# Performance work log

Hardware: AMD Instinct MI355X
Metric: run time of the kernel (lower is better)

## Reference

```python
import jax, jax.numpy as jnp
import numpy as np
import math

D_MODEL = 1024
N_HEADS = 16
HEAD_DIM = D_MODEL // N_HEADS
MAX_CONTEXT_LEN = 512


def _alibi_slopes(n_heads):
    def pow2_slopes(n):
        start = 2.0 ** (-(2.0 ** (-(math.log2(n) - 3))))
        return [start * (start ** i) for i in range(n)]
    if math.log2(n_heads).is_integer():
        slopes = pow2_slopes(n_heads)
    else:
        closest = 2 ** math.floor(math.log2(n_heads))
        slopes = pow2_slopes(closest)
        slopes += pow2_slopes(2 * closest)[0::2][: n_heads - closest]
    return jnp.asarray(slopes, dtype=jnp.float32)


def setup_inputs() -> dict:
    key = jax.random.key(0)
    ks = jax.random.split(key, 9)
    B, L, D = 4, 2048, D_MODEL
    s = 1.0 / math.sqrt(D)
    inp = {
        "x": jax.random.normal(ks[0], (B, L, D), dtype=jnp.float32),
        "key_padding_mask": jnp.zeros((B, L), dtype=bool),
        "Wq": jax.random.normal(ks[1], (D, D), dtype=jnp.float32) * s,
        "bq": jnp.zeros((D,), dtype=jnp.float32),
        "Wk": jax.random.normal(ks[2], (D, D), dtype=jnp.float32) * s,
        "bk": jnp.zeros((D,), dtype=jnp.float32),
        "Wv": jax.random.normal(ks[3], (D, D), dtype=jnp.float32) * s,
        "bv": jnp.zeros((D,), dtype=jnp.float32),
        "Wo": jax.random.normal(ks[4], (D, D), dtype=jnp.float32) * s,
        "bo": jnp.zeros((D,), dtype=jnp.float32),
    }
    return inp


def _attn(x, key_padding_mask, Wq, bq, Wk, bk, Wv, bv, Wo, bo):
    B, L, D = x.shape
    H, d = N_HEADS, HEAD_DIM
    # projections (torch Linear: x @ W.T + b)
    q = (x @ Wq.T + bq).reshape(B, L, H, d)
    k = (x @ Wk.T + bk).reshape(B, L, H, d)
    v = (x @ Wv.T + bv).reshape(B, L, H, d)
    scores = jnp.einsum("bihd,bjhd->bhij", q, k) / math.sqrt(d)  # (B,H,L,L)
    # ALiBi bias: slope[h] * (j - i)
    i = jnp.arange(L)[:, None]
    j = jnp.arange(L)[None, :]
    slopes = _alibi_slopes(H).astype(scores.dtype)
    scores = scores + slopes[None, :, None, None] * (j - i).astype(scores.dtype)
    # causal + sliding-window mask
    mask = (j > i) | (j < i - MAX_CONTEXT_LEN)
    neg_inf = jnp.asarray(-jnp.inf, dtype=scores.dtype)
    scores = jnp.where(mask[None, None, :, :], neg_inf, scores)
    scores = jnp.where(key_padding_mask[:, None, None, :], neg_inf, scores)
    attn = jax.nn.softmax(scores, axis=-1)
    out = jnp.einsum("bhij,bjhd->bihd", attn, v).reshape(B, L, D)
    return out @ Wo.T + bo


def reference(x, key_padding_mask, Wq, bq, Wk, bk, Wv, bv, Wo, bo):
    return _attn(x, key_padding_mask, Wq, bq, Wk, bk, Wv, bv, Wo, bo)
```

## Files before the change

kernel.cpp:

```cpp
#include <hip/hip_runtime.h>
#include <stdint.h>

typedef __attribute__((ext_vector_type(8))) short bf16x8;
typedef __attribute__((ext_vector_type(4))) short s16x4;
typedef __attribute__((ext_vector_type(4))) float f32x4;

#define MFMA_BF16(A, B, C) __builtin_amdgcn_mfma_f32_16x16x32_bf16((A), (B), (C), 0, 0, 0)

__device__ __forceinline__ float bf2f(short u) {
  union { unsigned u32; float f; } c; c.u32 = ((unsigned)(unsigned short)u) << 16; return c.f;
}
__device__ __forceinline__ short f2bf(float f) {
  union { float f; unsigned u32; } c; c.f = f;
  unsigned u = c.u32;
  return (short)((u + 0x7fffu + ((u >> 16) & 1u)) >> 16);
}
__device__ __forceinline__ short f2bf_t(float f) {
  union { float f; unsigned u32; } c; c.f = f;
  return (short)(c.u32 >> 16);
}

#define NEG_BIG (-30000.0f)

__device__ __forceinline__ void async16(const void* g, void* l) {
  __builtin_amdgcn_global_load_lds(
      (__attribute__((address_space(1))) void*)(g),
      (__attribute__((address_space(3))) void*)(l), 16, 0, 0);
}

__global__ void __launch_bounds__(256) convert_kernel(
    const float* __restrict__ X,
    const float* __restrict__ W0, const float* __restrict__ W1,
    const float* __restrict__ W2, const float* __restrict__ W3,
    const float* __restrict__ B0, const float* __restrict__ B1,
    const float* __restrict__ B2, const float* __restrict__ B3,
    short* __restrict__ Xb, short* __restrict__ Wb, short* __restrict__ bb)
{
  long c = (long)blockIdx.x * 256 + threadIdx.x;
  const float* src; short* dst; long off;
  if (c < 2097152) {
    src = X; dst = Xb; off = c * 4;
  } else if (c < 3145728) {
    long u = c - 2097152; int w = (int)(u >> 18);
    src = (w == 0) ? W0 : (w == 1) ? W1 : (w == 2) ? W2 : W3;
    dst = Wb + (long)w * 1048576; off = (u & 262143) * 4;
  } else {
    long u = c - 3145728; int w = (int)(u >> 8);
    src = (w == 0) ? B0 : (w == 1) ? B1 : (w == 2) ? B2 : B3;
    dst = bb + w * 1024; off = (u & 255) * 4;
  }
  float4 v = *(const float4*)(src + off);
  s16x4 o; o[0] = f2bf(v.x); o[1] = f2bf(v.y); o[2] = f2bf(v.z); o[3] = f2bf(v.w);
  *(s16x4*)(dst + off) = o;
}

#define STAGE_B(PG2, KK)                                                     \
  {                                                                          \
    short* sb_ = lds + (PG2) + PA + wave * 512;                              \
    async16(gB + (KK), sb_);                                                 \
    async16(gB + 65536 + (KK), sb_ + 2048);                                  \
  }
#define STAGE_A(PG2, KK)                                                     \
  {                                                                          \
    short* sa_ = lds + (PG2) + wave * 512;                                   \
    _Pragma("unroll")                                                        \
    for (int q = 0; q < AR; ++q)                                             \
      async16(gA + (long)q * 65536 + (KK), sa_ + q * 2048);                  \
  }
#define KTILE(PG, PG2, STG, KK2, VM)                                         \
  {                                                                          \
    const short* pa_ = lds + (PG);                                           \
    const short* pb_ = pa_ + PA;                                             \
    _Pragma("unroll")                                                        \
    for (int m = 0; m < MT; ++m) {                                           \
      int rA = wr * (MT * 16) + m * 16 + ml;                                 \
      af[m] = *(const bf16x8*)(pa_ + rA * 32 + sl);                          \
    }                                                                        \
    _Pragma("unroll")                                                        \
    for (int n = 0; n < 4; ++n) {                                            \
      int rB = wcn * 64 + n * 16 + ml;                                       \
      bf[n] = *(const bf16x8*)(pb_ + rB * 32 + sl);                          \
    }                                                                        \
    if (STG) { STAGE_B(PG2, KK2) STAGE_A(PG2, KK2) }                         \
    __builtin_amdgcn_s_setprio(1);                                           \
    _Pragma("unroll")                                                        \
    for (int m = 0; m < MT; ++m)                                             \
      _Pragma("unroll")                                                      \
      for (int n = 0; n < 4; ++n)                                            \
        acc[m][n] = MFMA_BF16(af[m], bf[n], acc[m][n]);                      \
    __builtin_amdgcn_s_setprio(0);                                           \
    if constexpr ((VM) == 1) {                                               \
      if constexpr (MT == 8)                                                 \
        asm volatile("s_waitcnt vmcnt(6)" ::: "memory");                     \
      else                                                                   \
        asm volatile("s_waitcnt vmcnt(4)" ::: "memory");                     \
    } else if constexpr ((VM) == 2) {                                        \
      asm volatile("s_waitcnt vmcnt(0)" ::: "memory");                       \
    }                                                                        \
    if constexpr ((VM) != 0) {                                               \
      __builtin_amdgcn_s_barrier();                                          \
      __builtin_amdgcn_sched_barrier(0);                                     \
    }                                                                        \
  }

template <int MODE, int MT>
__device__ __forceinline__ void gemm_body(
    short* __restrict__ lds,
    const short* __restrict__ A, const short* __restrict__ W,
    const short* __restrict__ bias, void* __restrict__ C,
    float scale, int row0, int col0)
{
  constexpr int PA   = MT * 1024;
  constexpr int PAGE = PA + 4096;
  constexpr int AR   = MT / 2;

  const int tid  = threadIdx.x;
  const int lane = tid & 63;
  const int wave = tid >> 6;
  const int wr   = wave >> 1;
  const int wcn  = wave & 1;
  const int ml = lane & 15, quad = lane >> 4;

  f32x4 acc[MT][4];
  const f32x4 zero = {0.f, 0.f, 0.f, 0.f};
#pragma unroll
  for (int i = 0; i < MT; ++i)
#pragma unroll
    for (int j = 0; j < 4; ++j) acc[i][j] = zero;

  const int r_l = tid >> 2;
  const int c_l = (tid & 3) ^ ((r_l >> 1) & 3);
  const short* gA = A + (long)(row0 + r_l) * 1024 + c_l * 8;
  const short* gB = W + (long)(col0 + r_l) * 1024 + c_l * 8;

  const int sl = (quad ^ ((ml >> 1) & 3)) << 3;

  bf16x8 af[MT], bf[4];

  STAGE_A(0, 0) STAGE_B(0, 0)
  STAGE_A(PAGE, 32) STAGE_B(PAGE, 32)
  if constexpr (MT == 8) asm volatile("s_waitcnt vmcnt(6)" ::: "memory");
  else                   asm volatile("s_waitcnt vmcnt(4)" ::: "memory");
  __builtin_amdgcn_s_barrier();
  __builtin_amdgcn_sched_barrier(0);

  for (int t = 0; t < 30; t += 3) {
    const long k2 = (long)(t + 2) * 32;
    KTILE(0,        2 * PAGE, true, k2,      1)
    KTILE(PAGE,     0,        true, k2 + 32, 1)
    KTILE(2 * PAGE, PAGE,     true, k2 + 64, 1)
  }
  KTILE(0,    0, false, 0, 2)
  KTILE(PAGE, 0, false, 0, 0)

  const int ccol = col0 + wcn * 64;
  float bv4[4];
#pragma unroll
  for (int nt = 0; nt < 4; ++nt) bv4[nt] = bf2f(bias[ccol + nt * 16 + ml]);

  if (MODE == 2) {
    const int b = row0 >> 11;
    short* Vt = (short*)C;
#pragma unroll
    for (int mt = 0; mt < MT; ++mt) {
      int rr = row0 + wr * (MT * 16) + mt * 16 + quad * 4;
      int tloc = rr & 2047;
#pragma unroll
      for (int nt = 0; nt < 4; ++nt) {
        int cc = ccol + nt * 16 + ml;
        int h = cc >> 6, d = cc & 63;
        s16x4 pack;
#pragma unroll
        for (int r = 0; r < 4; ++r) pack[r] = f2bf(acc[mt][nt][r] + bv4[nt]);
        *(s16x4*)(Vt + (long)(b * 16 + h) * 131072 + (long)d * 2048 + tloc) = pack;
      }
    }
  } else {
#pragma unroll
    for (int mt = 0; mt < MT; ++mt) {
      int rr = row0 + wr * (MT * 16) + mt * 16 + quad * 4;
#pragma unroll
      for (int nt = 0; nt < 4; ++nt) {
        int cc = ccol + nt * 16 + ml;
#pragma unroll
        for (int r = 0; r < 4; ++r) {
          float v = (acc[mt][nt][r] + bv4[nt]) * scale;
          long idx = (long)(rr + r) * 1024 + cc;
          if (MODE == 1) ((float*)C)[idx] = v;
          else           ((short*)C)[idx] = f2bf(v);
        }
      }
    }
  }
}
#undef KTILE
#undef STAGE_A
#undef STAGE_B

__global__ void __launch_bounds__(256, 2) qkv_kernel(
    const short* __restrict__ Xb, const short* __restrict__ Wb,
    const short* __restrict__ bb,
    short* __restrict__ Q, short* __restrict__ K, short* __restrict__ Vt,
    float qscale)
{
  __shared__ __align__(16) short lds[36864];
  const int z = blockIdx.z;
  const short* W = Wb + (long)z * 1048576;
  const short* b = bb + z * 1024;
  if (z == 2) {
    gemm_body<2, 8>(lds, Xb, W, b, Vt, 1.0f, blockIdx.x * 256, blockIdx.y * 128);
  } else {
    short* C = (z == 0) ? Q : K;
    float sc = (z == 0) ? qscale : 1.0f;
    gemm_body<0, 8>(lds, Xb, W, b, C, sc, blockIdx.x * 256, blockIdx.y * 128);
  }
}

__global__ void __launch_bounds__(256, 2) proj_kernel(
    const short* __restrict__ A, const short* __restrict__ Wb,
    const short* __restrict__ bb, float* __restrict__ Out)
{
  __shared__ __align__(16) short lds[24576];
  gemm_body<1, 4>(lds, A, Wb + (long)3 * 1048576, bb + 3 * 1024, Out,
                  1.0f, blockIdx.x * 128, blockIdx.y * 128);
}

#define ATTN_STAGE(KT, BUF)                                                  \
  {                                                                          \
    const int k0s_ = (KT) * 64;                                              \
    _Pragma("unroll")                                                        \
    for (int i_ = 0; i_ < 2; ++i_) {                                         \
      int ublk_ = wave * 2 + i_;                                             \
      int u_ = ublk_ * 64 + lane;                                            \
      int r_ = u_ >> 3, sg_ = u_ & 7;                                        \
      int sgg_ = sg_ ^ (r_ & 7);                                             \
      async16(Kb + (long)(k0s_ + r_) * 1024 + sgg_ * 8,                      \
              lK[BUF] + ublk_ * 512);                                        \
      async16(Vtb + (long)r_ * 2048 + k0s_ + sgg_ * 8,                       \
              lVt[BUF] + ublk_ * 512);                                       \
    }                                                                        \
  }

__global__ void __launch_bounds__(256) attn_kernel(
    const short* Q, const short* __restrict__ K,
    const short* __restrict__ Vt, short* O)
{
  const int id = blockIdx.x;
  const int bh = id & 63;
  const int qt = id >> 6;
  const int i0 = qt * 64;
  const int b  = bh >> 4;
  const int h  = bh & 15;
  const int tid = threadIdx.x;
  const int lane = tid & 63;
  const int wave = tid >> 6;
  const int ml = lane & 15, quad = lane >> 4;

  __shared__ __align__(16) short lK[2][64 * 64];
  __shared__ __align__(16) short lVt[2][64 * 64];
  __shared__ __align__(16) short lP[4][16 * 72];

  const float slope_l2 = exp2f(-0.5f * (float)(h + 1)) * 1.4426950408889634f;

  const int qrow = b * 2048 + i0 + wave * 16 + ml;
  bf16x8 qf[2];
  qf[0] = *(const bf16x8*)(Q + (long)qrow * 1024 + h * 64 + quad * 8);
  qf[1] = *(const bf16x8*)(Q + (long)qrow * 1024 + h * 64 + 32 + quad * 8);

  bf16x8 onesf;
#pragma unroll
  for (int j = 0; j < 8; ++j) onesf[j] = (short)0x3F80;

  f32x4 accO[4];
  f32x4 accL;
  const f32x4 zero = {0.f, 0.f, 0.f, 0.f};
#pragma unroll
  for (int i = 0; i < 4; ++i) accO[i] = zero;
  accL = zero;

  const int iq = i0 + wave * 16 + quad * 4;
  float browr[4];
#pragma unroll
  for (int r = 0; r < 4; ++r) browr[r] = slope_l2 * (float)(iq + r);

  const short* Kb  = K + (long)(b * 2048) * 1024 + h * 64;
  const short* Vtb = Vt + (long)bh * 131072;

  const int kt_lo = (i0 >= 512) ? ((i0 - 512) >> 6) : 0;
  const int kt_hi = i0 >> 6;

  ATTN_STAGE(kt_lo, kt_lo & 1)

  for (int kt = kt_lo; kt <= kt_hi; ++kt) {
    const int k0 = kt * 64;
    const int bufi = kt & 1;

    if (kt < kt_hi) {
      ATTN_STAGE(kt + 1, bufi ^ 1)
      asm volatile("s_waitcnt vmcnt(4)" ::: "memory");
    } else {
      asm volatile("s_waitcnt vmcnt(0)" ::: "memory");
    }
    __builtin_amdgcn_s_barrier();
    __builtin_amdgcn_sched_barrier(0);

    f32x4 s[4];
#pragma unroll
    for (int nt = 0; nt < 4; ++nt) s[nt] = zero;
#pragma unroll
    for (int nt = 0; nt < 4; ++nt) {
      int rB = nt * 16 + ml;
#pragma unroll
      for (int ks = 0; ks < 2; ++ks) {
        int seg = ks * 4 + quad;
        bf16x8 kf = *(const bf16x8*)(lK[bufi] + rB * 64 + ((seg ^ (rB & 7)) << 3));
        s[nt] = MFMA_BF16(qf[ks], kf, s[nt]);
      }
    }

    float bcol[4];
#pragma unroll
    for (int nt = 0; nt < 4; ++nt)
      bcol[nt] = slope_l2 * (float)(k0 + nt * 16 + ml);

    if (kt != kt_lo && kt != kt_hi) {
#pragma unroll
      for (int nt = 0; nt < 4; ++nt)
#pragma unroll
        for (int r = 0; r < 4; ++r) {
          float p = exp2f((s[nt][r] + bcol[nt]) - browr[r]);
          lP[wave][(quad * 4 + r) * 72 + nt * 16 + ml] = f2bf_t(p);
        }
    } else {
#pragma unroll
      for (int nt = 0; nt < 4; ++nt) {
        int j = k0 + nt * 16 + ml;
#pragma unroll
        for (int r = 0; r < 4; ++r) {
          int ii = iq + r;
          bool bad = (j > ii) || (j < ii - 512);
          float val = bad ? NEG_BIG : ((s[nt][r] + bcol[nt]) - browr[r]);
          lP[wave][(quad * 4 + r) * 72 + nt * 16 + ml] = f2bf_t(exp2f(val));
        }
      }
    }
    asm volatile("s_waitcnt lgkmcnt(0)" ::: "memory");

#pragma unroll
    for (int ks = 0; ks < 2; ++ks) {
      bf16x8 pf = *(const bf16x8*)(&lP[wave][ml * 72 + ks * 32 + quad * 8]);
      accL = MFMA_BF16(pf, onesf, accL);
#pragma unroll
      for (int d = 0; d < 4; ++d) {
        int drow = d * 16 + ml;
        int seg = ks * 4 + quad;
        bf16x8 vf = *(const bf16x8*)(lVt[bufi] + drow * 64 + ((seg ^ (drow & 7)) << 3));
        accO[d] = MFMA_BF16(pf, vf, accO[d]);
      }
    }

    __builtin_amdgcn_s_barrier();
    __builtin_amdgcn_sched_barrier(0);
  }

#pragma unroll
  for (int r = 0; r < 4; ++r) {
    float inv = 1.0f / accL[r];
    int orow = b * 2048 + i0 + wave * 16 + quad * 4 + r;
#pragma unroll
    for (int d = 0; d < 4; ++d)
      O[(long)orow * 1024 + h * 64 + d * 16 + ml] = f2bf(accO[d][r] * inv);
  }
}
#undef ATTN_STAGE

extern "C" void kernel_launch(void* const* d_in, const int* in_sizes, int n_in,
                              void* d_out, int out_size, void* d_ws, size_t ws_size,
                              hipStream_t stream) {
  const void* X = nullptr;
  const void* W[4] = {nullptr, nullptr, nullptr, nullptr};
  const void* Bs[4] = {nullptr, nullptr, nullptr, nullptr};
  int nw = 0, nb = 0;
  for (int i = 0; i < n_in; ++i) {
    int s = in_sizes[i];
    if (s == 1024 * 1024)          { if (nw < 4) W[nw++] = d_in[i]; }
    else if (s == 1024)            { if (nb < 4) Bs[nb++] = d_in[i]; }
    else if (s == 4 * 2048 * 1024) { if (!X) X = d_in[i]; }
  }

  char* ws = (char*)d_ws;
  short* Xb = (short*)(ws);
  short* Wb = (short*)(ws + (size_t)(16u << 20));
  short* bb = (short*)(ws + (size_t)(24u << 20));
  short* Q  = (short*)(ws + (size_t)(25u << 20));
  short* Kk = (short*)d_out;
  short* Vt = (short*)d_out + 8388608;
  short* AO = Q;

  const float qscale = 0.125f * 1.4426950408889634f;

  convert_kernel<<<12292, 256, 0, stream>>>(
      (const float*)X, (const float*)W[0], (const float*)W[1],
      (const float*)W[2], (const float*)W[3], (const float*)Bs[0],
      (const float*)Bs[1], (const float*)Bs[2], (const float*)Bs[3],
      Xb, Wb, bb);
  qkv_kernel<<<dim3(32, 8, 3), 256, 0, stream>>>(Xb, Wb, bb, Q, Kk, Vt, qscale);
  attn_kernel<<<2048, 256, 0, stream>>>(Q, Kk, Vt, AO);
  proj_kernel<<<dim3(64, 8), 256, 0, stream>>>(AO, Wb, bb, (float*)d_out);
}
```

Baseline: 225.7 us.

## Rewrite QKV projection as fused 128x384 tile GEMM with 512-thread blocks

```diff
diff --git a/kernel.cpp b/kernel.cpp
--- a/kernel.cpp
+++ b/kernel.cpp
@@ -54,6 +54,125 @@
   *(s16x4*)(dst + off) = o;
 }
 
+#define QSTAGE(PG, KK)                                                       \
+  {                                                                          \
+    short* sa_ = lds + (PG) + wave * 512;                                    \
+    async16(gA + (KK), sa_);                                                 \
+    short* sb_ = lds + (PG) + 4096 + wave * 512;                             \
+    async16(gB + (KK), sb_);                                                 \
+    async16(gB + 131072 + (KK), sb_ + 4096);                                 \
+    async16(gB + 262144 + (KK), sb_ + 8192);                                 \
+  }
+#define QKTILE(PG, PG2, STG, KK1, VM, TB)                                    \
+  {                                                                          \
+    if (STG) QSTAGE(PG2, KK1)                                                \
+    if ((VM) == 1) asm volatile("s_waitcnt vmcnt(4)" ::: "memory");          \
+    else           asm volatile("s_waitcnt vmcnt(0)" ::: "memory");          \
+    __builtin_amdgcn_s_barrier();                                            \
+    __builtin_amdgcn_sched_barrier(0);                                       \
+    const short* pa_ = lds + (PG);                                           \
+    const short* pb_ = pa_ + 4096;                                           \
+    bf16x8 af[4], bf[6];                                                     \
+    _Pragma("unroll")                                                        \
+    for (int m = 0; m < 4; ++m) {                                            \
+      int rA = wr * 64 + m * 16 + ml;                                        \
+      af[m] = *(const bf16x8*)(pa_ + rA * 32 + sl);                          \
+    }                                                                        \
+    _Pragma("unroll")                                                        \
+    for (int n = 0; n < 6; ++n) {                                            \
+      int rB = wcn * 96 + n * 16 + ml;                                       \
+      bf[n] = *(const bf16x8*)(pb_ + rB * 32 + sl);                          \
+    }                                                                        \
+    __builtin_amdgcn_s_setprio(1);                                           \
+    _Pragma("unroll")                                                        \
+    for (int m = 0; m < 4; ++m)                                              \
+      _Pragma("unroll")                                                      \
+      for (int n = 0; n < 6; ++n)                                            \
+        acc[m][n] = MFMA_BF16(af[m], bf[n], acc[m][n]);                      \
+    __builtin_amdgcn_s_setprio(0);                                           \
+    if (TB) {                                                                \
+      __builtin_amdgcn_s_barrier();                                          \
+      __builtin_amdgcn_sched_barrier(0);                                     \
+    }                                                                        \
+  }
+
+__global__ void __launch_bounds__(512, 2) qkv_kernel(
+    const short* __restrict__ Xb, const short* __restrict__ Wb,
+    const short* __restrict__ bb,
+    short* __restrict__ Q, short* __restrict__ K, short* __restrict__ Vt,
+    float qscale)
+{
+  __shared__ __align__(16) short lds[32768];
+  constexpr int PAGE = 16384;
+
+  const int tid  = threadIdx.x;
+  const int lane = tid & 63;
+  const int wave = tid >> 6;
+  const int wr   = wave >> 2;
+  const int wcn  = wave & 3;
+  const int ml = lane & 15, quad = lane >> 4;
+  const int row0 = blockIdx.x * 128;
+  const int col0 = blockIdx.y * 384;
+
+  f32x4 acc[4][6];
+  const f32x4 zero = {0.f, 0.f, 0.f, 0.f};
+#pragma unroll
+  for (int i = 0; i < 4; ++i)
+#pragma unroll
+    for (int j = 0; j < 6; ++j) acc[i][j] = zero;
+
+  const int r_l = tid >> 2;
+  const int c_l = (tid & 3) ^ ((r_l >> 1) & 3);
+  const short* gA = Xb + (long)(row0 + r_l) * 1024 + c_l * 8;
+  const short* gB = Wb + (long)(col0 + r_l) * 1024 + c_l * 8;
+
+  const int sl = (quad ^ ((ml >> 1) & 3)) << 3;
+
+  QSTAGE(0, 0)
+
+  for (int t = 0; t < 30; t += 2) {
+    QKTILE(0,    PAGE, true, (long)(t + 1) * 32, 1, 1)
+    QKTILE(PAGE, 0,    true, (long)(t + 2) * 32, 1, 1)
+  }
+  QKTILE(0,    PAGE, true,  (long)31 * 32, 1, 1)
+  QKTILE(PAGE, 0,    false, 0,             2, 0)
+
+  float bv[6];
+#pragma unroll
+  for (int n = 0; n < 6; ++n)
+    bv[n] = bf2f(bb[col0 + wcn * 96 + n * 16 + ml]);
+
+  const int bb_ = row0 >> 11;
+#pragma unroll
+  for (int mt = 0; mt < 4; ++mt) {
+    int rr = row0 + wr * 64 + mt * 16 + quad * 4;
+    int tloc = rr & 2047;
+#pragma unroll
+    for (int nt = 0; nt < 6; ++nt) {
+      int cc = col0 + wcn * 96 + nt * 16 + ml;
+      int zsel = cc >> 10;
+      int cloc = cc & 1023;
+      if (zsel == 0) {
+#pragma unroll
+        for (int r = 0; r < 4; ++r)
+          Q[(long)(rr + r) * 1024 + cloc] = f2bf((acc[mt][nt][r] + bv[nt]) * qscale);
+      } else if (zsel == 1) {
+#pragma unroll
+        for (int r = 0; r < 4; ++r)
+          K[(long)(rr + r) * 1024 + cloc] = f2bf(acc[mt][nt][r] + bv[nt]);
+      } else {
+        int h = cloc >> 6, d = cloc & 63;
+        s16x4 pack;
+#pragma unroll
+        for (int r = 0; r < 4; ++r) pack[r] = f2bf(acc[mt][nt][r] + bv[nt]);
+        *(s16x4*)(Vt + (long)(bb_ * 16 + h) * 131072 + (long)d * 2048 + tloc) = pack;
+      }
+    }
+  }
+}
+#undef QKTILE
+#undef QSTAGE
+
 #define STAGE_B(PG2, KK)                                                     \
   {                                                                          \
     short* sb_ = lds + (PG2) + PA + wave * 512;                              \
@@ -90,10 +209,7 @@
         acc[m][n] = MFMA_BF16(af[m], bf[n], acc[m][n]);                      \
     __builtin_amdgcn_s_setprio(0);                                           \
     if constexpr ((VM) == 1) {                                               \
-      if constexpr (MT == 8)                                                 \
-        asm volatile("s_waitcnt vmcnt(6)" ::: "memory");                     \
-      else                                                                   \
-        asm volatile("s_waitcnt vmcnt(4)" ::: "memory");                     \
+      asm volatile("s_waitcnt vmcnt(4)" ::: "memory");                       \
     } else if constexpr ((VM) == 2) {                                        \
       asm volatile("s_waitcnt vmcnt(0)" ::: "memory");                       \
     }                                                                        \
@@ -132,15 +248,13 @@
   const int c_l = (tid & 3) ^ ((r_l >> 1) & 3);
   const short* gA = A + (long)(row0 + r_l) * 1024 + c_l * 8;
   const short* gB = W + (long)(col0 + r_l) * 1024 + c_l * 8;
-
   const int sl = (quad ^ ((ml >> 1) & 3)) << 3;
 
   bf16x8 af[MT], bf[4];
 
   STAGE_A(0, 0) STAGE_B(0, 0)
   STAGE_A(PAGE, 32) STAGE_B(PAGE, 32)
-  if constexpr (MT == 8) asm volatile("s_waitcnt vmcnt(6)" ::: "memory");
-  else                   asm volatile("s_waitcnt vmcnt(4)" ::: "memory");
+  asm volatile("s_waitcnt vmcnt(4)" ::: "memory");
   __builtin_amdgcn_s_barrier();
   __builtin_amdgcn_sched_barrier(0);
 
@@ -158,37 +272,18 @@
 #pragma unroll
   for (int nt = 0; nt < 4; ++nt) bv4[nt] = bf2f(bias[ccol + nt * 16 + ml]);
 
-  if (MODE == 2) {
-    const int b = row0 >> 11;
-    short* Vt = (short*)C;
-#pragma unroll
-    for (int mt = 0; mt < MT; ++mt) {
-      int rr = row0 + wr * (MT * 16) + mt * 16 + quad * 4;
-      int tloc = rr & 2047;
-#pragma unroll
-      for (int nt = 0; nt < 4; ++nt) {
-        int cc = ccol + nt * 16 + ml;
-        int h = cc >> 6, d = cc & 63;
-        s16x4 pack;
-#pragma unroll
-        for (int r = 0; r < 4; ++r) pack[r] = f2bf(acc[mt][nt][r] + bv4[nt]);
-        *(s16x4*)(Vt + (long)(b * 16 + h) * 131072 + (long)d * 2048 + tloc) = pack;
-      }
-    }
-  } else {
-#pragma unroll
-    for (int mt = 0; mt < MT; ++mt) {
-      int rr = row0 + wr * (MT * 16) + mt * 16 + quad * 4;
-#pragma unroll
-      for (int nt = 0; nt < 4; ++nt) {
-        int cc = ccol + nt * 16 + ml;
-#pragma unroll
-        for (int r = 0; r < 4; ++r) {
-          float v = (acc[mt][nt][r] + bv4[nt]) * scale;
-          long idx = (long)(rr + r) * 1024 + cc;
-          if (MODE == 1) ((float*)C)[idx] = v;
-          else           ((short*)C)[idx] = f2bf(v);
-        }
+#pragma unroll
+  for (int mt = 0; mt < MT; ++mt) {
+    int rr = row0 + wr * (MT * 16) + mt * 16 + quad * 4;
+#pragma unroll
+    for (int nt = 0; nt < 4; ++nt) {
+      int cc = ccol + nt * 16 + ml;
+#pragma unroll
+      for (int r = 0; r < 4; ++r) {
+        float v = (acc[mt][nt][r] + bv4[nt]) * scale;
+        long idx = (long)(rr + r) * 1024 + cc;
+        if (MODE == 1) ((float*)C)[idx] = v;
+        else           ((short*)C)[idx] = f2bf(v);
       }
     }
   }
@@ -196,25 +291,6 @@
 #undef KTILE
 #undef STAGE_A
 #undef STAGE_B
-
-__global__ void __launch_bounds__(256, 2) qkv_kernel(
-    const short* __restrict__ Xb, const short* __restrict__ Wb,
-    const short* __restrict__ bb,
-    short* __restrict__ Q, short* __restrict__ K, short* __restrict__ Vt,
-    float qscale)
-{
-  __shared__ __align__(16) short lds[36864];
-  const int z = blockIdx.z;
-  const short* W = Wb + (long)z * 1048576;
-  const short* b = bb + z * 1024;
-  if (z == 2) {
-    gemm_body<2, 8>(lds, Xb, W, b, Vt, 1.0f, blockIdx.x * 256, blockIdx.y * 128);
-  } else {
-    short* C = (z == 0) ? Q : K;
-    float sc = (z == 0) ? qscale : 1.0f;
-    gemm_body<0, 8>(lds, Xb, W, b, C, sc, blockIdx.x * 256, blockIdx.y * 128);
-  }
-}
 
 __global__ void __launch_bounds__(256, 2) proj_kernel(
     const short* __restrict__ A, const short* __restrict__ Wb,
@@ -404,7 +480,7 @@
       (const float*)W[2], (const float*)W[3], (const float*)Bs[0],
       (const float*)Bs[1], (const float*)Bs[2], (const float*)Bs[3],
       Xb, Wb, bb);
-  qkv_kernel<<<dim3(32, 8, 3), 256, 0, stream>>>(Xb, Wb, bb, Q, Kk, Vt, qscale);
+  qkv_kernel<<<dim3(64, 8), 512, 0, stream>>>(Xb, Wb, bb, Q, Kk, Vt, qscale);
   attn_kernel<<<2048, 256, 0, stream>>>(Q, Kk, Vt, AO);
   proj_kernel<<<dim3(64, 8), 256, 0, stream>>>(AO, Wb, bb, (float*)d_out);
 }
```

Measured after the change: 227.5 us. Within noise of the previous version (+0.8%).
